# Kernel optimization log

Hardware: AMD Instinct MI355X
Metric: run time of the kernel (lower is better)

Reference implementation:

```python
import jax, jax.numpy as jnp
import numpy as np

N_EMBD = 1024
N_HEAD = 16
HEAD_DIM = N_EMBD // N_HEAD
WINDOW = 256


def setup_inputs() -> dict:
    key = jax.random.key(0)
    ks = jax.random.split(key, 9)
    B, T, C = 2, 2048, N_EMBD
    s = 1.0 / np.sqrt(C)
    inp = {
        'x': jax.random.normal(ks[0], (B, T, C), jnp.float32),
        'Wq': jax.random.normal(ks[1], (C, C), jnp.float32) * s,
        'bq': jnp.zeros((C,), jnp.float32),
        'Wk': jax.random.normal(ks[2], (C, C), jnp.float32) * s,
        'bk': jnp.zeros((C,), jnp.float32),
        'Wv': jax.random.normal(ks[3], (C, C), jnp.float32) * s,
        'bv': jnp.zeros((C,), jnp.float32),
        'Wo': jax.random.normal(ks[4], (C, C), jnp.float32) * s,
        'bo': jnp.zeros((C,), jnp.float32),
    }
    return inp


def reference(x, Wq, bq, Wk, bk, Wv, bv, Wo, bo):
    B, T, C = x.shape
    H, D = N_HEAD, HEAD_DIM
    # projections -> [B, H, T, D]
    q = (x @ Wq + bq).reshape(B, T, H, D).transpose(0, 2, 1, 3)
    k = (x @ Wk + bk).reshape(B, T, H, D).transpose(0, 2, 1, 3)
    v = (x @ Wv + bv).reshape(B, T, H, D).transpose(0, 2, 1, 3)
    # dense scores [B, H, T, T]
    scores = jnp.einsum('bhid,bhjd->bhij', q, k) / jnp.sqrt(jnp.float32(D))
    # sliding-window + causal mask: allow j <= i and i - j <= WINDOW
    i = jnp.arange(T)[:, None]
    j = jnp.arange(T)[None, :]
    mask = (j <= i) & (i - j <= WINDOW)  # [T, T]
    scores = jnp.where(mask[None, None], scores, -jnp.inf)
    probs = jax.nn.softmax(scores, axis=-1)
    out = jnp.einsum('bhij,bhjd->bhid', probs, v)  # [B,H,T,D]
    out = out.transpose(0, 2, 1, 3).reshape(B, T, C)
    return out @ Wo + bo
```

## Files before the change

kernel.cpp:

```cpp
#include <hip/hip_runtime.h>


typedef _Float16 f16;
typedef _Float16 half8 __attribute__((ext_vector_type(8)));
typedef _Float16 half4 __attribute__((ext_vector_type(4)));
typedef float    f32x4 __attribute__((ext_vector_type(4)));

#define MFMA16(a, b, c) __builtin_amdgcn_mfma_f32_16x16x32_f16((a), (b), (c), 0, 0, 0)

__device__ __forceinline__ void gload16(const void* g, void* l) {
  __builtin_amdgcn_global_load_lds(
      (const __attribute__((address_space(1))) void*)g,
      (__attribute__((address_space(3))) void*)l, 16, 0, 0);
}

__global__ __launch_bounds__(256) void prep_kernel(
    const float* __restrict__ x, f16* __restrict__ xb,
    const float* __restrict__ W0, const float* __restrict__ W1,
    const float* __restrict__ W2, const float* __restrict__ W3,
    f16* __restrict__ T0, f16* __restrict__ T1,
    f16* __restrict__ T2, f16* __restrict__ T3) {
  const int bid = blockIdx.x;
  if (bid < 2048) {
    const int idx = (bid * 256 + threadIdx.x) * 8;
    const float4 a = *(const float4*)(x + idx);
    const float4 b = *(const float4*)(x + idx + 4);
    half8 h;
    h[0] = (f16)a.x; h[1] = (f16)a.y; h[2] = (f16)a.z; h[3] = (f16)a.w;
    h[4] = (f16)b.x; h[5] = (f16)b.y; h[6] = (f16)b.z; h[7] = (f16)b.w;
    *(half8*)(xb + idx) = h;
    return;
  }
  __shared__ float tile[32][33];
  const int rem0 = bid - 2048;
  const int mat = rem0 >> 10;
  const int rem = rem0 & 1023;
  const int kt = (rem >> 5) * 32;
  const int nt = (rem & 31) * 32;
  const float* W = mat == 0 ? W0 : mat == 1 ? W1 : mat == 2 ? W2 : W3;
  f16* T = mat == 0 ? T0 : mat == 1 ? T1 : mat == 2 ? T2 : T3;
  const int tid = threadIdx.x;
  const int r = tid >> 3;
  const int c4 = (tid & 7) * 4;
  const float4 v = *(const float4*)(W + (size_t)(kt + r) * 1024 + nt + c4);
  tile[r][c4 + 0] = v.x; tile[r][c4 + 1] = v.y;
  tile[r][c4 + 2] = v.z; tile[r][c4 + 3] = v.w;
  __syncthreads();
  if (tid < 128) {
    const int n = tid >> 2;
    const int k8 = (tid & 3) * 8;
    half8 o;
    #pragma unroll
    for (int e = 0; e < 8; e++) o[e] = (f16)tile[k8 + e][n];
    *(half8*)(T + (size_t)(nt + n) * 1024 + kt + k8) = o;
  }
}

__device__ __forceinline__ void gemm_core4(const f16* __restrict__ A,
                                           const f16* __restrict__ Bt,
                                           int m0, int n0,
                                           f16* As, f16* Bs,
                                           f32x4 acc[4][4]) {
  const int tid = threadIdx.x;
  const int lane = tid & 63, wave = tid >> 6;
  const int wm = wave >> 1, wn = wave & 1;
  const int fr = lane & 15, fg = lane >> 4;
  const int sx = (fr & 7) << 4;

  const int srow = wave * 32 + (lane >> 3);
  const int cc = lane & 7;
  const size_t go = (size_t)srow * 1024 + (size_t)((cc ^ (srow & 7)) * 8);
  const f16* ag = A + (size_t)m0 * 1024 + go;
  const f16* bg = Bt + (size_t)n0 * 1024 + go;
  f16* la = As + wave * 2048;
  f16* lb = Bs + wave * 2048;

  #pragma unroll
  for (int i = 0; i < 4; i++)
    #pragma unroll
    for (int j = 0; j < 4; j++) acc[i][j] = (f32x4){0.f, 0.f, 0.f, 0.f};

  for (int kt = 0; kt < 1024; kt += 64) {
    #pragma unroll
    for (int t = 0; t < 4; t++) {
      gload16(ag + kt + t * 8192, la + t * 512);
      gload16(bg + kt + t * 8192, lb + t * 512);
    }
    __syncthreads();
    const char* Ab = (const char*)As;
    const char* Bb = (const char*)Bs;
    #pragma unroll
    for (int kk = 0; kk < 2; kk++) {
      half8 af[4], bf[4];
      const int co = (kk * 64 + fg * 16) ^ sx;
      #pragma unroll
      for (int mf = 0; mf < 4; mf++)
        af[mf] = *(const half8*)(Ab + (wm * 64 + mf * 16 + fr) * 128 + co);
      #pragma unroll
      for (int nf = 0; nf < 4; nf++)
        bf[nf] = *(const half8*)(Bb + (wn * 64 + nf * 16 + fr) * 128 + co);
      #pragma unroll
      for (int mf = 0; mf < 4; mf++)
        #pragma unroll
        for (int nf = 0; nf < 4; nf++)
          acc[mf][nf] = MFMA16(af[mf], bf[nf], acc[mf][nf]);
    }
    __syncthreads();
  }
}

__global__ __launch_bounds__(256, 3) void gemm_qkv_kernel(
    const f16* __restrict__ xb, const f16* __restrict__ wt,
    const float* __restrict__ bq, const float* __restrict__ bk,
    const float* __restrict__ bv,
    f16* __restrict__ qo, f16* __restrict__ ko, f16* __restrict__ vt) {
  __shared__ __align__(16) f16 As[128 * 64];
  __shared__ __align__(16) f16 Bs[128 * 64];
  const int wg = (blockIdx.x & 7) * 96 + (blockIdx.x >> 3);
  const int m0 = (wg & 31) * 128;
  const int n0 = (wg >> 5) * 128;
  f32x4 acc[4][4];
  gemm_core4(xb, wt, m0, n0, As, Bs, acc);

  const int lane = threadIdx.x & 63, wave = threadIdx.x >> 6;
  const int wm = wave >> 1, wn = wave & 1;
  const int fr = lane & 15, fg = lane >> 4;
  const int matid = n0 >> 10;
  const int nc0 = n0 & 1023;
  const float* bias = matid == 0 ? bq : matid == 1 ? bk : bv;
  if (matid < 2) {
    f16* out = matid == 0 ? qo : ko;
    #pragma unroll
    for (int mf = 0; mf < 4; mf++)
      #pragma unroll
      for (int nf = 0; nf < 4; nf++) {
        const int col = nc0 + wn * 64 + nf * 16 + fr;
        const float bb = bias[col];
        #pragma unroll
        for (int r = 0; r < 4; r++) {
          const int row = m0 + wm * 64 + mf * 16 + fg * 4 + r;
          out[(size_t)row * 1024 + col] = (f16)(acc[mf][nf][r] + bb);
        }
      }
  } else {
    #pragma unroll
    for (int mf = 0; mf < 4; mf++)
      #pragma unroll
      for (int nf = 0; nf < 4; nf++) {
        const int row = m0 + wm * 64 + mf * 16 + fg * 4;
        const int col = nc0 + wn * 64 + nf * 16 + fr;
        const int b = row >> 11, t = row & 2047;
        const int h = col >> 6, d = col & 63;
        const float bb = bias[col];
        half4 vv;
        #pragma unroll
        for (int r = 0; r < 4; r++) vv[r] = (f16)(acc[mf][nf][r] + bb);
        *(half4*)(vt + (((size_t)(b * 16 + h)) * 64 + d) * 2048 + t) = vv;
      }
  }
}

__global__ __launch_bounds__(256, 4) void gemm_o_kernel(
    const f16* __restrict__ ao, const f16* __restrict__ wot,
    const float* __restrict__ bo, float* __restrict__ out) {
  __shared__ __align__(16) f16 As[128 * 64];
  __shared__ __align__(16) f16 Bs[64 * 64];
  const int wg = (blockIdx.x & 7) * 64 + (blockIdx.x >> 3);
  const int m0 = (wg & 31) * 128;
  const int n0 = (wg >> 5) * 64;

  const int tid = threadIdx.x;
  const int lane = tid & 63, wave = tid >> 6;
  const int wm = wave >> 1, wn = wave & 1;
  const int fr = lane & 15, fg = lane >> 4;
  const int sx = (fr & 7) << 4;

  const int cc = lane & 7;
  const int srA = wave * 32 + (lane >> 3);
  const int srB = wave * 16 + (lane >> 3);
  const size_t goA = (size_t)srA * 1024 + (size_t)((cc ^ (srA & 7)) * 8);
  const size_t goB = (size_t)srB * 1024 + (size_t)((cc ^ (srB & 7)) * 8);
  const f16* ag = ao + (size_t)m0 * 1024 + goA;
  const f16* bg = wot + (size_t)n0 * 1024 + goB;
  f16* la = As + wave * 2048;
  f16* lb = Bs + wave * 1024;

  f32x4 acc[4][2];
  #pragma unroll
  for (int i = 0; i < 4; i++)
    #pragma unroll
    for (int j = 0; j < 2; j++) acc[i][j] = (f32x4){0.f, 0.f, 0.f, 0.f};

  for (int kt = 0; kt < 1024; kt += 64) {
    #pragma unroll
    for (int t = 0; t < 4; t++) gload16(ag + kt + t * 8192, la + t * 512);
    #pragma unroll
    for (int t = 0; t < 2; t++) gload16(bg + kt + t * 8192, lb + t * 512);
    __syncthreads();
    const char* Ab = (const char*)As;
    const char* Bb = (const char*)Bs;
    #pragma unroll
    for (int kk = 0; kk < 2; kk++) {
      half8 af[4], bf[2];
      const int co = (kk * 64 + fg * 16) ^ sx;
      #pragma unroll
      for (int mf = 0; mf < 4; mf++)
        af[mf] = *(const half8*)(Ab + (wm * 64 + mf * 16 + fr) * 128 + co);
      #pragma unroll
      for (int nf = 0; nf < 2; nf++)
        bf[nf] = *(const half8*)(Bb + (wn * 32 + nf * 16 + fr) * 128 + co);
      #pragma unroll
      for (int mf = 0; mf < 4; mf++)
        #pragma unroll
        for (int nf = 0; nf < 2; nf++)
          acc[mf][nf] = MFMA16(af[mf], bf[nf], acc[mf][nf]);
    }
    __syncthreads();
  }

  #pragma unroll
  for (int mf = 0; mf < 4; mf++)
    #pragma unroll
    for (int nf = 0; nf < 2; nf++) {
      const int col = n0 + wn * 32 + nf * 16 + fr;
      const float bb = bo[col];
      #pragma unroll
      for (int r = 0; r < 4; r++) {
        const int row = m0 + wm * 64 + mf * 16 + fg * 4 + r;
        out[(size_t)row * 1024 + col] = acc[mf][nf][r] + bb;
      }
    }
}

__global__ __launch_bounds__(256, 3) void attn_kernel(
    const f16* __restrict__ Q, const f16* __restrict__ K,
    const f16* __restrict__ Vt, f16* __restrict__ Ao) {
  __shared__ __align__(16) f16 Ks[2][64 * 64];
  __shared__ __align__(16) f16 Vs[2][64 * 64];
  __shared__ __align__(16) f16 Ps[4][32][72];

  const int tid = threadIdx.x, lane = tid & 63, wave = tid >> 6;
  const int fr = lane & 15, g = lane >> 4;
  const int wg = (blockIdx.x & 7) * 64 + (blockIdx.x >> 3);
  const int qt = wg & 15, bh = wg >> 4;
  const int b = bh >> 4, h = bh & 15;
  const int q0 = qt * 128;
  const int qr = q0 + wave * 32;

  const f16* Qb = Q + ((size_t)(b * 2048 + qr)) * 1024 + h * 64;
  half8 qf[2][2];
  #pragma unroll
  for (int mc = 0; mc < 2; mc++)
    #pragma unroll
    for (int kk = 0; kk < 2; kk++)
      qf[mc][kk] =
          *(const half8*)(Qb + (size_t)(mc * 16 + fr) * 1024 + kk * 32 + g * 8);

  const char* Kg = (const char*)(K + ((size_t)(b * 2048)) * 1024 + h * 64);
  const char* Vg = (const char*)(Vt + ((size_t)(b * 16 + h)) * 64 * 2048);

  const int sr = wave * 16 + (lane >> 3);
  const int sco = ((lane & 7) ^ (sr & 7)) << 4;

  auto stageKV = [&](int buf, int jt) {
    #pragma unroll
    for (int t = 0; t < 2; t++) {
      gload16(Kg + (size_t)(jt + sr + t * 8) * 2048 + sco,
              (f16*)Ks[buf] + wave * 1024 + t * 512);
      gload16(Vg + (size_t)(sr + t * 8) * 4096 + (size_t)jt * 2 + sco,
              (f16*)Vs[buf] + wave * 1024 + t * 512);
    }
  };

  const int t0 = q0 >= 256 ? (q0 - 256) >> 6 : 0;
  const int t1 = (q0 + 127) >> 6;

  f32x4 O[2][4];
  #pragma unroll
  for (int mc = 0; mc < 2; mc++)
    #pragma unroll
    for (int nt = 0; nt < 4; nt++) O[mc][nt] = (f32x4){0.f, 0.f, 0.f, 0.f};
  float lsum[2][4] = {{0.f, 0.f, 0.f, 0.f}, {0.f, 0.f, 0.f, 0.f}};

  stageKV(0, t0 * 64);
  __syncthreads();

  for (int tt = t0; tt <= t1; ++tt) {
    const int cur = (tt - t0) & 1;
    if (tt < t1) stageKV(cur ^ 1, (tt + 1) * 64);
    const int jt = tt * 64;
    const bool alive = (jt <= qr + 31) && (jt + 63 >= qr - 256);
    if (alive) {
      const char* Kb = (const char*)Ks[cur];
      const char* Vb = (const char*)Vs[cur];
      f32x4 s[2][4];
      #pragma unroll
      for (int jj = 0; jj < 4; ++jj) {
        const int kj = jj * 16 + fr;
        const char* krow = Kb + kj * 128;
        const int kswz = (kj & 7) << 4;
        const half8 kf0 = *(const half8*)(krow + ((g * 16) ^ kswz));
        const half8 kf1 = *(const half8*)(krow + ((64 + g * 16) ^ kswz));
        #pragma unroll
        for (int mc = 0; mc < 2; mc++) {
          f32x4 z = (f32x4){0.f, 0.f, 0.f, 0.f};
          z = MFMA16(qf[mc][0], kf0, z);
          z = MFMA16(qf[mc][1], kf1, z);
          s[mc][jj] = z;
        }
      }
      #pragma unroll
      for (int mc = 0; mc < 2; mc++) {
        const int eb = qr + mc * 16 + g * 4 - jt - fr;
        #pragma unroll
        for (int jj = 0; jj < 4; ++jj) {
          #pragma unroll
          for (int r = 0; r < 4; ++r) {
            const float a = __expf(s[mc][jj][r] * 0.125f - 3.0f);
            const float p = ((unsigned)(eb + r - jj * 16) <= 256u) ? a : 0.f;
            lsum[mc][r] += p;
            Ps[wave][mc * 16 + g * 4 + r][jj * 16 + fr] = (f16)p;
          }
        }
      }
      #pragma unroll
      for (int ks = 0; ks < 2; ++ks) {
        const half8 pa0 = *(const half8*)(&Ps[wave][fr][ks * 32 + g * 8]);
        const half8 pa1 = *(const half8*)(&Ps[wave][16 + fr][ks * 32 + g * 8]);
        #pragma unroll
        for (int nt = 0; nt < 4; ++nt) {
          const int vd = nt * 16 + fr;
          const half8 vf = *(const half8*)(
              Vb + vd * 128 + ((ks * 64 + g * 16) ^ ((vd & 7) << 4)));
          O[0][nt] = MFMA16(pa0, vf, O[0][nt]);
          O[1][nt] = MFMA16(pa1, vf, O[1][nt]);
        }
      }
    }
    __syncthreads();
  }

  float inv[2][4];
  #pragma unroll
  for (int mc = 0; mc < 2; mc++)
    #pragma unroll
    for (int r = 0; r < 4; ++r) {
      float s = lsum[mc][r];
      s += __shfl_xor(s, 1);
      s += __shfl_xor(s, 2);
      s += __shfl_xor(s, 4);
      s += __shfl_xor(s, 8);
      inv[mc][r] = 1.0f / s;
    }
  f16* Aout = Ao + ((size_t)(b * 2048 + qr)) * 1024 + h * 64;
  #pragma unroll
  for (int mc = 0; mc < 2; mc++)
    #pragma unroll
    for (int nt = 0; nt < 4; ++nt)
      #pragma unroll
      for (int r = 0; r < 4; ++r)
        Aout[(size_t)(mc * 16 + g * 4 + r) * 1024 + nt * 16 + fr] =
            (f16)(O[mc][nt][r] * inv[mc][r]);
}

extern "C" void kernel_launch(void* const* d_in, const int* in_sizes, int n_in,
                              void* d_out, int out_size, void* d_ws,
                              size_t ws_size, hipStream_t stream) {
  const float* x  = (const float*)d_in[0];
  const float* Wq = (const float*)d_in[1];
  const float* bq = (const float*)d_in[2];
  const float* Wk = (const float*)d_in[3];
  const float* bk = (const float*)d_in[4];
  const float* Wv = (const float*)d_in[5];
  const float* bv = (const float*)d_in[6];
  const float* Wo = (const float*)d_in[7];
  const float* bo = (const float*)d_in[8];

  char* w = (char*)d_ws;
  f16* xb  = (f16*)(w);
  f16* wqt = (f16*)(w + ((size_t)8 << 20));
  f16* wkt = (f16*)(w + ((size_t)10 << 20));
  f16* wvt = (f16*)(w + ((size_t)12 << 20));
  f16* wot = (f16*)(w + ((size_t)14 << 20));
  f16* q   = (f16*)(w + ((size_t)16 << 20));
  f16* kk  = (f16*)(w + ((size_t)24 << 20));
  f16* vt  = (f16*)(w + ((size_t)32 << 20));
  f16* ao  = (f16*)(w + ((size_t)40 << 20));

  prep_kernel<<<6144, 256, 0, stream>>>(x, xb, Wq, Wk, Wv, Wo,
                                        wqt, wkt, wvt, wot);
  gemm_qkv_kernel<<<768, 256, 0, stream>>>(xb, wqt, bq, bk, bv, q, kk, vt);
  attn_kernel<<<512, 256, 0, stream>>>(q, kk, vt, ao);
  gemm_o_kernel<<<512, 256, 0, stream>>>(ao, wot, bo, (float*)d_out);
}
```

Baseline: 79.41 us.

## Keep attention probabilities in registers by computing transposed scores

Computes S^T (K as the A operand, Q as B) so each lane's score outputs line up with the A-operand layout of the PV MFMA, and packs the probabilities straight into half8 registers. This removes the per-wave shared-memory Ps buffer along with its writes and reads. V fragments are now assembled from two half4 LDS reads with a permuted k ordering that matches the new P layout. Row sums are reduced across lane groups and redistributed with shuffles. The risk is a mismatch in the k-index permutation, and the split V loads use more LDS instructions.

```diff
diff --git a/kernel.cpp b/kernel.cpp
--- a/kernel.cpp
+++ b/kernel.cpp
@@ -237,7 +237,6 @@
     const f16* __restrict__ Vt, f16* __restrict__ Ao) {
   __shared__ __align__(16) f16 Ks[2][64 * 64];
   __shared__ __align__(16) f16 Vs[2][64 * 64];
-  __shared__ __align__(16) f16 Ps[4][32][72];
 
   const int tid = threadIdx.x, lane = tid & 63, wave = tid >> 6;
   const int fr = lane & 15, g = lane >> 4;
@@ -280,7 +279,7 @@
   for (int mc = 0; mc < 2; mc++)
     #pragma unroll
     for (int nt = 0; nt < 4; nt++) O[mc][nt] = (f32x4){0.f, 0.f, 0.f, 0.f};
-  float lsum[2][4] = {{0.f, 0.f, 0.f, 0.f}, {0.f, 0.f, 0.f, 0.f}};
+  float lsum[2] = {0.f, 0.f};
 
   stageKV(0, t0 * 64);
   __syncthreads();
@@ -293,7 +292,7 @@
     if (alive) {
       const char* Kb = (const char*)Ks[cur];
       const char* Vb = (const char*)Vs[cur];
-      f32x4 s[2][4];
+      half8 pa[2][2];
       #pragma unroll
       for (int jj = 0; jj < 4; ++jj) {
         const int kj = jj * 16 + fr;
@@ -302,38 +301,35 @@
         const half8 kf0 = *(const half8*)(krow + ((g * 16) ^ kswz));
         const half8 kf1 = *(const half8*)(krow + ((64 + g * 16) ^ kswz));
         #pragma unroll
-        for (int mc = 0; mc < 2; mc++) {
+        for (int mc = 0; mc < 2; ++mc) {
           f32x4 z = (f32x4){0.f, 0.f, 0.f, 0.f};
-          z = MFMA16(qf[mc][0], kf0, z);
-          z = MFMA16(qf[mc][1], kf1, z);
-          s[mc][jj] = z;
-        }
-      }
-      #pragma unroll
-      for (int mc = 0; mc < 2; mc++) {
-        const int eb = qr + mc * 16 + g * 4 - jt - fr;
-        #pragma unroll
-        for (int jj = 0; jj < 4; ++jj) {
+          z = MFMA16(kf0, qf[mc][0], z);
+          z = MFMA16(kf1, qf[mc][1], z);
+          const int eb = qr + mc * 16 + fr - jt - jj * 16 - g * 4;
           #pragma unroll
           for (int r = 0; r < 4; ++r) {
-            const float a = __expf(s[mc][jj][r] * 0.125f - 3.0f);
-            const float p = ((unsigned)(eb + r - jj * 16) <= 256u) ? a : 0.f;
-            lsum[mc][r] += p;
-            Ps[wave][mc * 16 + g * 4 + r][jj * 16 + fr] = (f16)p;
+            const float a = __expf(z[r] * 0.125f - 3.0f);
+            const float p = ((unsigned)(eb - r) <= 256u) ? a : 0.f;
+            lsum[mc] += p;
+            pa[mc][jj >> 1][(jj & 1) * 4 + r] = (f16)p;
           }
         }
       }
       #pragma unroll
       for (int ks = 0; ks < 2; ++ks) {
-        const half8 pa0 = *(const half8*)(&Ps[wave][fr][ks * 32 + g * 8]);
-        const half8 pa1 = *(const half8*)(&Ps[wave][16 + fr][ks * 32 + g * 8]);
         #pragma unroll
         for (int nt = 0; nt < 4; ++nt) {
           const int vd = nt * 16 + fr;
-          const half8 vf = *(const half8*)(
-              Vb + vd * 128 + ((ks * 64 + g * 16) ^ ((vd & 7) << 4)));
-          O[0][nt] = MFMA16(pa0, vf, O[0][nt]);
-          O[1][nt] = MFMA16(pa1, vf, O[1][nt]);
+          const int sw = (vd & 7) << 4;
+          const half4 vlo =
+              *(const half4*)(Vb + vd * 128 + ((ks * 64 + 8 * g) ^ sw));
+          const half4 vhi =
+              *(const half4*)(Vb + vd * 128 + ((ks * 64 + 32 + 8 * g) ^ sw));
+          half8 vf;
+          vf[0] = vlo[0]; vf[1] = vlo[1]; vf[2] = vlo[2]; vf[3] = vlo[3];
+          vf[4] = vhi[0]; vf[5] = vhi[1]; vf[6] = vhi[2]; vf[7] = vhi[3];
+          O[0][nt] = MFMA16(pa[0][ks], vf, O[0][nt]);
+          O[1][nt] = MFMA16(pa[1][ks], vf, O[1][nt]);
         }
       }
     }
@@ -342,19 +338,16 @@
 
   float inv[2][4];
   #pragma unroll
-  for (int mc = 0; mc < 2; mc++)
-    #pragma unroll
-    for (int r = 0; r < 4; ++r) {
-      float s = lsum[mc][r];
-      s += __shfl_xor(s, 1);
-      s += __shfl_xor(s, 2);
-      s += __shfl_xor(s, 4);
-      s += __shfl_xor(s, 8);
-      inv[mc][r] = 1.0f / s;
-    }
+  for (int mc = 0; mc < 2; ++mc) {
+    float t = lsum[mc];
+    t += __shfl_xor(t, 16);
+    t += __shfl_xor(t, 32);
+    #pragma unroll
+    for (int r = 0; r < 4; ++r) inv[mc][r] = 1.0f / __shfl(t, g * 4 + r);
+  }
   f16* Aout = Ao + ((size_t)(b * 2048 + qr)) * 1024 + h * 64;
   #pragma unroll
-  for (int mc = 0; mc < 2; mc++)
+  for (int mc = 0; mc < 2; ++mc)
     #pragma unroll
     for (int nt = 0; nt < 4; ++nt)
       #pragma unroll
```

After: 78.69 us. No clear change (-0.9%).
